# Performance work log

Measured on AMD Instinct MI355X. Metric: run time of the kernel, lower is better.

Reference implementation:

```python
import jax, jax.numpy as jnp
import numpy as np

SC = 11  # window stride / block size; unfold kernel = 3*SC = 33, padding = SC


def _unfold3(x, sc):
    """Equivalent of nn.Unfold(kernel=3*sc, stride=sc, padding=sc) on [b,c,H,W]
    where H, W are multiples of sc. Returns [b, c, 9*sc*sc, n_windows].
    Patch ordering within K differs from torch by a fixed permutation, which is
    immaterial: all contractions over K (mask, softmax, value aggregation) are
    permutation-invariant as long as the same unfold is used everywhere."""
    b, c, H, W = x.shape
    h_sc, w_sc = H // sc, W // sc
    xp = jnp.pad(x, ((0, 0), (0, 0), (sc, sc), (sc, sc)))
    blk = xp.reshape(b, c, h_sc + 2, sc, w_sc + 2, sc)
    # 3x3 neighborhood of sc-blocks around each window
    pat = jnp.stack([blk[:, :, di:di + h_sc, :, dj:dj + w_sc, :]
                     for di in range(3) for dj in range(3)], axis=2)
    # [b,c,9,h_sc,r,w_sc,s] -> [b,c,9,r,s,h_sc,w_sc] -> [b,c,9*sc*sc,n]
    pat = pat.transpose(0, 1, 2, 4, 6, 3, 5)
    return pat.reshape(b, c, 9 * sc * sc, h_sc * w_sc)


def _block_q(x, sc):
    """view(b,c,h_sc,sc,w_sc,sc).permute(0,1,2,4,3,5) -> [b,c,n,sc*sc]"""
    b, c, H, W = x.shape
    h_sc, w_sc = H // sc, W // sc
    y = x.reshape(b, c, h_sc, sc, w_sc, sc).transpose(0, 1, 2, 4, 3, 5)
    return y.reshape(b, c, h_sc * w_sc, sc * sc)


def setup_inputs() -> dict:
    key = jax.random.key(0)
    k1, k2, k3, k4, k5, k6 = jax.random.split(key, 6)
    b, c, h, w = 2, 64, 256, 256
    s = 1.0 / np.sqrt(c)
    return {
        "x_key": jax.random.normal(k1, (b, c, h, w), jnp.float32),
        "x_ref": jax.random.normal(k2, (b, c, h, w), jnp.float32),
        "Wq": jax.random.normal(k3, (c, c), jnp.float32) * s,
        "Wk": jax.random.normal(k4, (c, c), jnp.float32) * s,
        "Wv": jax.random.normal(k5, (c, c), jnp.float32) * s,
        "gamma": jax.random.normal(k6, (1,), jnp.float32) * 0.1,
    }


def reference(x_key, x_ref, Wq, Wk, Wv, gamma):
    sc = SC
    b, c, h_in, w_in = x_key.shape
    x_pad = sc - w_in % sc
    y_pad = sc - h_in % sc
    pad = ((0, 0), (0, 0), (0, y_pad), (0, x_pad))
    fk = jnp.pad(x_key, pad)
    fr = jnp.pad(x_ref, pad)
    b, c, h, w = fk.shape
    h_sc, w_sc = h // sc, w // sc

    # validity mask -> additive attention bias (out-of-image keys penalized)
    fm = jnp.pad(jnp.ones((1, 1, h_in, w_in), fk.dtype), pad)
    fm_k = _unfold3(fm, sc)          # [1,1,K,n]
    fm_q = _block_q(fm, sc)          # [1,1,n,s]
    am = (jnp.einsum('bckn,bcns->bkns', fm_k, fm_q) - 1.0) * 99.0  # [1,K,n,s]

    scale = c ** (-0.5)
    q = jnp.einsum('oi,bihw->bohw', Wq, fk)
    k = jnp.einsum('oi,bihw->bohw', Wk, fr)
    v = jnp.einsum('oi,bihw->bohw', Wv, fr)

    k_u = _unfold3(k, sc) * scale    # [b,c,K,n]
    q_b = _block_q(q, sc)            # [b,c,n,s]
    attn = jnp.einsum('bckn,bcns->bkns', k_u, q_b) + am  # [b,K,n,s]
    attn = jax.nn.softmax(attn, axis=1)

    v_u = _unfold3(v, sc)            # [b,c,K,n]
    r = jnp.einsum('bkns,bckn->bcns', attn, v_u)  # [b,c,n,s]
    r = r.reshape(b, c, h_sc, w_sc, sc, sc).transpose(0, 1, 2, 4, 3, 5)
    r = r.reshape(b, c, h, w)[:, :, :h_in, :w_in]
    return x_ref + r * gamma[0]
```

## Files before the change

### kernel.cpp

```cpp
#include <hip/hip_runtime.h>


typedef unsigned short ushort_t;
typedef unsigned int   uint32;
typedef unsigned long long uint64;
typedef __attribute__((ext_vector_type(8))) short short8;
typedef __attribute__((ext_vector_type(4))) float f32x4;

#define MFMA16(a,b,c) __builtin_amdgcn_mfma_f32_16x16x32_bf16(a,b,c,0,0,0)

#if __has_builtin(__builtin_amdgcn_exp2f)
#define EXP2(x) __builtin_amdgcn_exp2f(x)
#else
#define EXP2(x) exp2f(x)
#endif
#if __has_builtin(__builtin_amdgcn_rcpf)
#define RCP(x) __builtin_amdgcn_rcpf(x)
#else
#define RCP(x) (1.0f/(x))
#endif

#define QPKT_OFF   0u
#define KPKT_OFF   18874368u
#define VPKT_OFF   37748736u

__device__ __forceinline__ ushort_t f2bf(float f){
  uint32 u = __float_as_uint(f);
  u = (u + 0x7FFFu + ((u >> 16) & 1u)) >> 16;
  return (ushort_t)u;
}

__device__ __forceinline__ uint32 pkbf(float a, float b){
#if __has_builtin(__builtin_amdgcn_cvt_pk_bf16_f32)
  typedef __attribute__((ext_vector_type(2))) __bf16 bf2;
  union { bf2 v; uint32 u; } c;
  c.v = __builtin_amdgcn_cvt_pk_bf16_f32(a, b);
  return c.u;
#else
  return (uint32)f2bf(a) | ((uint32)f2bf(b) << 16);
#endif
}

__device__ __forceinline__ void storeK8(ushort_t* __restrict__ base, int nt, int t,
                                        int l15, int h, f32x4 a){
  uint32 lo = pkbf(a[0], a[1]);
  uint32 hi = pkbf(a[2], a[3]);
  int lanep = l15 + 16*((2*t + (h>>1)) & 3);
  size_t off = (size_t)((nt*2 + (t>>1))*64 + lanep)*16 + 8*(h&1);
  *(uint2*)((char*)base + off) = make_uint2(lo, hi);
}

__device__ __forceinline__ short8 ldWfrag(const float* __restrict__ W, int t, int ks,
                                          int l15, int h, float scale){
  const float* p = W + (16*t + l15)*64 + 32*ks + 8*h;
  float4 a = *(const float4*)p;
  float4 b = *(const float4*)(p + 4);
  union { uint4 u; short8 s; } x;
  x.u.x = pkbf(a.x*scale, a.y*scale);
  x.u.y = pkbf(a.z*scale, a.w*scale);
  x.u.z = pkbf(b.x*scale, b.y*scale);
  x.u.w = pkbf(b.z*scale, b.w*scale);
  return x.s;
}

__global__ __launch_bounds__(256) void proj_kernel(
    const float* __restrict__ xk, const float* __restrict__ xr,
    const float* __restrict__ Wq, const float* __restrict__ Wk, const float* __restrict__ Wv,
    ushort_t* __restrict__ qpkt, ushort_t* __restrict__ kpkt, ushort_t* __restrict__ vpkt)
{
  __shared__ __align__(16) float sX[64*192];
  const int tid = threadIdx.x;
  const int lane = tid & 63, wv = tid >> 6;
  const int l15 = lane & 15, h = lane >> 4;
  const int bid = blockIdx.x;
  const bool isQ = bid >= 1152;
  const int id = isQ ? bid - 1152 : bid;
  const int b = id / 576, rem = id % 576, ty = rem / 24, tx = rem % 24;
  const float* xs = (isQ ? xk : xr) + (size_t)b*64*65536;
  const int oy = ty*11, ox = tx*11;
  const int ox3 = ox & 3, xa = ox - ox3;

  #pragma unroll
  for (int i = tid; i < 1024; i += 256) sX[(i>>4)*192 + 176 + (i&15)] = 0.f;

  {
    const int ch = tid >> 2, seg = tid & 3;
    const float* rowp = xs + (size_t)ch*65536 + (size_t)oy*256 + (xa + 4*seg);
    float* sdst = sX + ch*192 + 4*seg;
    if (ty < 23 && tx < 23){
      #pragma unroll
      for (int y = 0; y < 11; ++y)
        *(float4*)(sdst + y*16) = *(const float4*)(rowp + y*256);
    } else {
      const int xg = xa + 4*seg;
      #pragma unroll
      for (int y = 0; y < 11; ++y){
        const bool rk = (oy + y) < 256;
        float4 v;
        v.x = (rk && xg+0 < 256) ? rowp[y*256+0] : 0.f;
        v.y = (rk && xg+1 < 256) ? rowp[y*256+1] : 0.f;
        v.z = (rk && xg+2 < 256) ? rowp[y*256+2] : 0.f;
        v.w = (rk && xg+3 < 256) ? rowp[y*256+3] : 0.f;
        *(float4*)(sdst + y*16) = v;
      }
    }
  }
  __syncthreads();

  const f32x4 zero = {0.f, 0.f, 0.f, 0.f};
  #define XFL(nt, ks, dst) { \
    const int px_ = 16*(nt) + l15; \
    const int y_ = (px_*745) >> 13; \
    const float* pp_ = sX + (32*(ks) + 8*h)*192 + y_*16 + (px_ - y_*11) + ox3; \
    union { uint4 u; short8 s; } r_; \
    r_.u.x = pkbf(pp_[0],    pp_[192]); \
    r_.u.y = pkbf(pp_[384],  pp_[576]); \
    r_.u.z = pkbf(pp_[768],  pp_[960]); \
    r_.u.w = pkbf(pp_[1152], pp_[1344]); \
    dst = r_.s; }

  if (!isQ){
    short8 wkf[4][2], wvf[4][2];
    #pragma unroll
    for (int t = 0; t < 4; ++t){
      wkf[t][0] = ldWfrag(Wk, t, 0, l15, h, 1.f);  wkf[t][1] = ldWfrag(Wk, t, 1, l15, h, 1.f);
      wvf[t][0] = ldWfrag(Wv, t, 0, l15, h, 1.f);  wvf[t][1] = ldWfrag(Wv, t, 1, l15, h, 1.f);
    }
    ushort_t* kb = kpkt + (size_t)id*8192;
    ushort_t* vb = vpkt + (size_t)id*8192;
    const int nt0 = 2*wv, nt1 = 2*wv + 1;
    short8 xf0[2], xf1[2];
    XFL(nt0, 0, xf0[0]); XFL(nt0, 1, xf0[1]);
    XFL(nt1, 0, xf1[0]); XFL(nt1, 1, xf1[1]);
    #pragma unroll
    for (int t = 0; t < 4; ++t){
      f32x4 ak0 = MFMA16(wkf[t][0], xf0[0], zero); ak0 = MFMA16(wkf[t][1], xf0[1], ak0);
      f32x4 ak1 = MFMA16(wkf[t][0], xf1[0], zero); ak1 = MFMA16(wkf[t][1], xf1[1], ak1);
      f32x4 av0 = MFMA16(xf0[0], wvf[t][0], zero); av0 = MFMA16(xf0[1], wvf[t][1], av0);
      f32x4 av1 = MFMA16(xf1[0], wvf[t][0], zero); av1 = MFMA16(xf1[1], wvf[t][1], av1);
      storeK8(kb, nt0, t, l15, h, ak0);
      storeK8(kb, nt1, t, l15, h, ak1);
      uint4 pv;
      pv.x = pkbf(av0[0], av0[1]); pv.y = pkbf(av0[2], av0[3]);
      pv.z = pkbf(av1[0], av1[1]); pv.w = pkbf(av1[2], av1[3]);
      *(uint4*)((char*)vb + (size_t)((wv*4 + t)*64 + lane)*16) = pv;
    }
  } else {
    const float C1 = 0.18033688011112042f;
    short8 wqf[4][2];
    #pragma unroll
    for (int t = 0; t < 4; ++t){
      wqf[t][0] = ldWfrag(Wq, t, 0, l15, h, C1);  wqf[t][1] = ldWfrag(Wq, t, 1, l15, h, C1);
    }
    ushort_t* qb = qpkt + (size_t)id*8192;
    #pragma unroll
    for (int nn = 0; nn < 2; ++nn){
      const int nt = 2*wv + nn;
      short8 xf[2];
      XFL(nt, 0, xf[0]); XFL(nt, 1, xf[1]);
      #pragma unroll
      for (int t = 0; t < 4; ++t){
        f32x4 aq = MFMA16(wqf[t][0], xf[0], zero); aq = MFMA16(wqf[t][1], xf[1], aq);
        storeK8(qb, nt, t, l15, h, aq);
      }
    }
  }
  #undef XFL
}

__global__ __launch_bounds__(128) void attn_kernel(
    ushort_t* qpkt,
    const ushort_t* __restrict__ kpkt, const ushort_t* __restrict__ vpkt,
    const float* __restrict__ gamma)
{
  __shared__ __align__(16) char smem[32768];
  const int tid = threadIdx.x;
  const int lane = tid & 63, wave = tid >> 6;
  const int win = (blockIdx.x & 7)*144 + (blockIdx.x >> 3);
  const int b = win / 576, wid = win % 576, wy = wid / 24, wx = wid % 24;
  const int l15 = lane & 15, h = lane >> 4;

  short8 qf[4][2];
  {
    const ushort_t* qblk = qpkt + (size_t)win*8192;
    #pragma unroll
    for (int mt = 0; mt < 4; ++mt){
      qf[mt][0] = *(const short8*)(qblk + (size_t)(((4*wave+mt)*2 + 0)*64 + lane)*8);
      qf[mt][1] = *(const short8*)(qblk + (size_t)(((4*wave+mt)*2 + 1)*64 + lane)*8);
    }
  }

  uint64 cks = 0; int nv = 0;
  #pragma unroll
  for (int ck = 0; ck < 9; ++ck){
    const int ty = wy - 1 + ck/3, tx = wx - 1 + ck%3;
    if ((unsigned)ty < 24u && (unsigned)tx < 24u){
      cks |= ((uint64)ck) << (4*nv); ++nv;
    }
  }
  const int nu = 2*nv;

  f32x4 o[4][4];
  float lsum[4] = {0.f, 0.f, 0.f, 0.f};
  #pragma unroll
  for (int mt = 0; mt < 4; ++mt)
    #pragma unroll
    for (int u = 0; u < 4; ++u) o[mt][u] = (f32x4){0.f,0.f,0.f,0.f};
  const f32x4 zz = {0.f,0.f,0.f,0.f};

  const ushort_t* gsrcbase = wave ? vpkt : kpkt;
  const int ldsw = wave ? 8192 : 0;

  #define STAGE(u, bu) { \
    const int t_ = (u) >> 1, hf_ = (u) & 1; \
    const int ck_ = (int)((cks >> (4*t_)) & 15); \
    const int cy_ = (ck_*11) >> 5; \
    const int ty_ = wy - 1 + cy_, tx_ = wx - 1 + (ck_ - 3*cy_); \
    const char* g_ = (const char*)(gsrcbase + (size_t)(b*576 + ty_*24 + tx_)*8192) \
                     + hf_*8192 + lane*16; \
    char* l_ = smem + (bu)*16384 + ldsw; \
    _Pragma("unroll") \
    for (int i_ = 0; i_ < 8; ++i_) \
      __builtin_amdgcn_global_load_lds( \
        (const __attribute__((address_space(1))) uint32*)(g_ + i_*1024), \
        (__attribute__((address_space(3))) uint32*)(l_ + i_*1024), 16, 0, 0); \
  }

  STAGE(0, 0);
  STAGE(1, 1);

  #pragma unroll 1
  for (int u = 0; u < nu; ++u){
    const int bu = u & 1;
    if (u + 1 < nu) { __asm__ volatile("s_waitcnt vmcnt(8)" ::: "memory"); }
    else            { __asm__ volatile("s_waitcnt vmcnt(0)" ::: "memory"); }
    __builtin_amdgcn_s_barrier();
    __asm__ volatile("" ::: "memory");

    const int t = u >> 1, hf = u & 1;
    const int ckv = (int)((cks >> (4*t)) & 15);
    const int cyv = (ckv*11) >> 5;
    const int tyv = wy - 1 + cyv, txv = wx - 1 + (ckv - 3*cyv);
    const bool ey = (tyv == 23), ex = (txv == 23);
    const char* lk = smem + bu*16384;
    const char* lv = lk + 8192;

    #pragma unroll
    for (int ntpl = 0; ntpl < 2; ++ntpl){
      const int ntp = 2*hf + ntpl;
      short8 kf00 = *(const short8*)(lk + ((4*ntpl+0)*64 + lane)*16);
      short8 kf01 = *(const short8*)(lk + ((4*ntpl+1)*64 + lane)*16);
      short8 kf10 = *(const short8*)(lk + ((4*ntpl+2)*64 + lane)*16);
      short8 kf11 = *(const short8*)(lk + ((4*ntpl+3)*64 + lane)*16);
      short8 vf0  = *(const short8*)(lv + ((4*ntpl+0)*64 + lane)*16);
      short8 vf1  = *(const short8*)(lv + ((4*ntpl+1)*64 + lane)*16);
      short8 vf2  = *(const short8*)(lv + ((4*ntpl+2)*64 + lane)*16);
      short8 vf3  = *(const short8*)(lv + ((4*ntpl+3)*64 + lane)*16);

      bool okk[8];
      #pragma unroll
      for (int kt = 0; kt < 2; ++kt)
        #pragma unroll
        for (int r = 0; r < 4; ++r){
          const int kl = 32*ntp + 16*kt + 4*h + r;
          bool ok = kl < 121;
          if (ey | ex){
            const int ky = (kl*745) >> 13, kx = kl - ky*11;
            if (ey) ok = ok && (ky < 3);
            if (ex) ok = ok && (kx < 3);
          }
          okk[4*kt + r] = ok;
        }

      #pragma unroll
      for (int mt = 0; mt < 4; ++mt){
        f32x4 s0 = MFMA16(kf00, qf[mt][0], zz); s0 = MFMA16(kf01, qf[mt][1], s0);
        f32x4 s1 = MFMA16(kf10, qf[mt][0], zz); s1 = MFMA16(kf11, qf[mt][1], s1);
        float p[8];
        #pragma unroll
        for (int r = 0; r < 4; ++r){
          p[r]   = okk[r]   ? EXP2(s0[r]) : 0.f;
          p[4+r] = okk[4+r] ? EXP2(s1[r]) : 0.f;
        }
        lsum[mt] += ((p[0]+p[1]) + (p[2]+p[3])) + ((p[4]+p[5]) + (p[6]+p[7]));
        union { uint4 uu; short8 s; } af;
        af.uu.x = pkbf(p[0], p[1]); af.uu.y = pkbf(p[2], p[3]);
        af.uu.z = pkbf(p[4], p[5]); af.uu.w = pkbf(p[6], p[7]);
        o[mt][0] = MFMA16(af.s, vf0, o[mt][0]);
        o[mt][1] = MFMA16(af.s, vf1, o[mt][1]);
        o[mt][2] = MFMA16(af.s, vf2, o[mt][2]);
        o[mt][3] = MFMA16(af.s, vf3, o[mt][3]);
      }
    }

    __asm__ volatile("" ::: "memory");
    __builtin_amdgcn_s_barrier();
    if (u + 2 < nu) STAGE(u + 2, bu);
  }
  #undef STAGE

  const float gm = gamma[0];
  ushort_t* rb = qpkt + (size_t)win*8192 + (size_t)wave*4096;
  #pragma unroll
  for (int mt = 0; mt < 4; ++mt){
    float v = lsum[mt];
    v += __shfl_xor(v, 16); v += __shfl_xor(v, 32);
    #pragma unroll
    for (int r = 0; r < 4; ++r){
      const float den = __shfl(v, 4*h + r);
      const float wg = gm * RCP(den);
      const int qs = 16*mt + 4*h + r;
      #pragma unroll
      for (int u = 0; u < 4; ++u)
        rb[(size_t)qs*64 + 16*u + l15] = f2bf(wg * o[mt][u][r]);
    }
  }
}

__global__ __launch_bounds__(256) void ep_kernel(
    const float* __restrict__ xref, const ushort_t* __restrict__ rbuf,
    float* __restrict__ out)
{
  __shared__ float tile[64][65];
  const int tid = threadIdx.x;
  const int bidx = blockIdx.x;
  const int xc = bidx & 3, y = (bidx >> 2) & 255, b = bidx >> 10;
  const int wy = (y*745) >> 13, qy = y - wy*11;
  {
    const int ch = tid & 63, xs4 = tid >> 6;
    #pragma unroll
    for (int xi = 0; xi < 16; ++xi){
      const int xl = xi*4 + xs4;
      const int x = xc*64 + xl;
      const int wx = (x*745) >> 13, qx = x - wx*11;
      const size_t ridx = (size_t)(b*576 + wy*24 + wx)*8192 + (size_t)(qy*11 + qx)*64 + ch;
      tile[xl][ch] = __uint_as_float(((uint32)rbuf[ridx]) << 16);
    }
  }
  __syncthreads();
  {
    const int xl = tid & 63, cg = tid >> 6;
    const size_t base = (size_t)b*4194304 + (size_t)y*256 + xc*64 + xl;
    #pragma unroll
    for (int ci = 0; ci < 16; ++ci){
      const int c2 = ci*4 + cg;
      const size_t idx = base + (size_t)c2*65536;
      out[idx] = xref[idx] + tile[xl][c2];
    }
  }
}

extern "C" void kernel_launch(void* const* d_in, const int* in_sizes, int n_in,
                              void* d_out, int out_size, void* d_ws, size_t ws_size,
                              hipStream_t stream)
{
  const float* xk = (const float*)d_in[0];
  const float* xr = (const float*)d_in[1];
  const float* Wq = (const float*)d_in[2];
  const float* Wk = (const float*)d_in[3];
  const float* Wv = (const float*)d_in[4];
  const float* gm = (const float*)d_in[5];
  float* out = (float*)d_out;
  char* ws = (char*)d_ws;
  ushort_t* qp = (ushort_t*)(ws + QPKT_OFF);
  ushort_t* kp = (ushort_t*)(ws + KPKT_OFF);
  ushort_t* vp = (ushort_t*)(ws + VPKT_OFF);
  (void)in_sizes; (void)n_in; (void)out_size; (void)ws_size;

  proj_kernel<<<2304, 256, 0, stream>>>(xk, xr, Wq, Wk, Wv, qp, kp, vp);
  attn_kernel<<<1152, 128, 0, stream>>>(qp, kp, vp, gm);
  ep_kernel<<<2048, 256, 0, stream>>>(xr, qp, out);
}
```

Before: 251.1 us.

## Split attention key tiles across four waves and reduce partial outputs via LDS

The attention kernel moves from 2 to 4 waves per window. Each wave pair handles half of the query rows and half of the key sub-tiles per stage, and the partial outputs and row sums are merged through shared memory at the end. The validity mask becomes an additive bias fed in as the MFMA accumulator init, and row sums are computed with an extra MFMA against a ones vector instead of scalar adds. This aims to raise latency hiding and cut per-wave VALU work, at the cost of an extra LDS reduction with several block barriers and an additional MFMA per tile.

```diff
diff --git a/kernel.cpp b/kernel.cpp
--- a/kernel.cpp
+++ b/kernel.cpp
@@ -168,7 +168,7 @@
   #undef XFL
 }
 
-__global__ __launch_bounds__(128) void attn_kernel(
+__global__ __launch_bounds__(256) void attn_kernel(
     ushort_t* qpkt,
     const ushort_t* __restrict__ kpkt, const ushort_t* __restrict__ vpkt,
     const float* __restrict__ gamma)
@@ -176,6 +176,7 @@
   __shared__ __align__(16) char smem[32768];
   const int tid = threadIdx.x;
   const int lane = tid & 63, wave = tid >> 6;
+  const int qh = wave & 1, kh = wave >> 1;
   const int win = (blockIdx.x & 7)*144 + (blockIdx.x >> 3);
   const int b = win / 576, wid = win % 576, wy = wid / 24, wx = wid % 24;
   const int l15 = lane & 15, h = lane >> 4;
@@ -185,8 +186,8 @@
     const ushort_t* qblk = qpkt + (size_t)win*8192;
     #pragma unroll
     for (int mt = 0; mt < 4; ++mt){
-      qf[mt][0] = *(const short8*)(qblk + (size_t)(((4*wave+mt)*2 + 0)*64 + lane)*8);
-      qf[mt][1] = *(const short8*)(qblk + (size_t)(((4*wave+mt)*2 + 1)*64 + lane)*8);
+      qf[mt][0] = *(const short8*)(qblk + (size_t)(((4*qh+mt)*2 + 0)*64 + lane)*8);
+      qf[mt][1] = *(const short8*)(qblk + (size_t)(((4*qh+mt)*2 + 1)*64 + lane)*8);
     }
   }
 
@@ -200,27 +201,34 @@
   }
   const int nu = 2*nv;
 
-  f32x4 o[4][4];
-  float lsum[4] = {0.f, 0.f, 0.f, 0.f};
+  const f32x4 zz = {0.f,0.f,0.f,0.f};
+  f32x4 o[4][4], lsumC[4];
   #pragma unroll
-  for (int mt = 0; mt < 4; ++mt)
-    #pragma unroll
-    for (int u = 0; u < 4; ++u) o[mt][u] = (f32x4){0.f,0.f,0.f,0.f};
-  const f32x4 zz = {0.f,0.f,0.f,0.f};
-
-  const ushort_t* gsrcbase = wave ? vpkt : kpkt;
-  const int ldsw = wave ? 8192 : 0;
+  for (int mt = 0; mt < 4; ++mt){
+    lsumC[mt] = zz;
+    #pragma unroll
+    for (int u = 0; u < 4; ++u) o[mt][u] = zz;
+  }
+  f32x4 init_i;
+  #pragma unroll
+  for (int r = 0; r < 4; ++r) init_i[r] = (4*h + r >= 9) ? -1.0e4f : 0.f;
+  short8 ones;
+  #pragma unroll
+  for (int j = 0; j < 8; ++j) ones[j] = (short)0x3F80;
+
+  const ushort_t* gsrc = (wave < 2) ? kpkt : vpkt;
+  const int ldsoff = (wave >> 1)*8192 + (wave & 1)*4096;
 
   #define STAGE(u, bu) { \
     const int t_ = (u) >> 1, hf_ = (u) & 1; \
     const int ck_ = (int)((cks >> (4*t_)) & 15); \
     const int cy_ = (ck_*11) >> 5; \
     const int ty_ = wy - 1 + cy_, tx_ = wx - 1 + (ck_ - 3*cy_); \
-    const char* g_ = (const char*)(gsrcbase + (size_t)(b*576 + ty_*24 + tx_)*8192) \
-                     + hf_*8192 + lane*16; \
-    char* l_ = smem + (bu)*16384 + ldsw; \
+    const char* g_ = (const char*)(gsrc + (size_t)(b*576 + ty_*24 + tx_)*8192) \
+                     + hf_*8192 + (wave & 1)*4096 + lane*16; \
+    char* l_ = smem + (bu)*16384 + ldsoff + lane*16; \
     _Pragma("unroll") \
-    for (int i_ = 0; i_ < 8; ++i_) \
+    for (int i_ = 0; i_ < 4; ++i_) \
       __builtin_amdgcn_global_load_lds( \
         (const __attribute__((address_space(1))) uint32*)(g_ + i_*1024), \
         (__attribute__((address_space(3))) uint32*)(l_ + i_*1024), 16, 0, 0); \
@@ -232,7 +240,7 @@
   #pragma unroll 1
   for (int u = 0; u < nu; ++u){
     const int bu = u & 1;
-    if (u + 1 < nu) { __asm__ volatile("s_waitcnt vmcnt(8)" ::: "memory"); }
+    if (u + 1 < nu) { __asm__ volatile("s_waitcnt vmcnt(4)" ::: "memory"); }
     else            { __asm__ volatile("s_waitcnt vmcnt(0)" ::: "memory"); }
     __builtin_amdgcn_s_barrier();
     __asm__ volatile("" ::: "memory");
@@ -242,55 +250,56 @@
     const int cyv = (ckv*11) >> 5;
     const int tyv = wy - 1 + cyv, txv = wx - 1 + (ckv - 3*cyv);
     const bool ey = (tyv == 23), ex = (txv == 23);
-    const char* lk = smem + bu*16384;
-    const char* lv = lk + 8192;
-
-    #pragma unroll
-    for (int ntpl = 0; ntpl < 2; ++ntpl){
-      const int ntp = 2*hf + ntpl;
-      short8 kf00 = *(const short8*)(lk + ((4*ntpl+0)*64 + lane)*16);
-      short8 kf01 = *(const short8*)(lk + ((4*ntpl+1)*64 + lane)*16);
-      short8 kf10 = *(const short8*)(lk + ((4*ntpl+2)*64 + lane)*16);
-      short8 kf11 = *(const short8*)(lk + ((4*ntpl+3)*64 + lane)*16);
-      short8 vf0  = *(const short8*)(lv + ((4*ntpl+0)*64 + lane)*16);
-      short8 vf1  = *(const short8*)(lv + ((4*ntpl+1)*64 + lane)*16);
-      short8 vf2  = *(const short8*)(lv + ((4*ntpl+2)*64 + lane)*16);
-      short8 vf3  = *(const short8*)(lv + ((4*ntpl+3)*64 + lane)*16);
-
-      bool okk[8];
-      #pragma unroll
-      for (int kt = 0; kt < 2; ++kt)
+    const int ntp = 2*hf + kh;
+
+    f32x4 b0, b1;
+    if (ey | ex){
+      #pragma unroll
+      for (int kt = 0; kt < 2; ++kt){
+        f32x4 bb;
         #pragma unroll
         for (int r = 0; r < 4; ++r){
           const int kl = 32*ntp + 16*kt + 4*h + r;
-          bool ok = kl < 121;
-          if (ey | ex){
-            const int ky = (kl*745) >> 13, kx = kl - ky*11;
-            if (ey) ok = ok && (ky < 3);
-            if (ex) ok = ok && (kx < 3);
-          }
-          okk[4*kt + r] = ok;
+          const int ky = (kl*745) >> 13, kx = kl - ky*11;
+          bool ok = (kl < 121) && (!ey || ky < 3) && (!ex || kx < 3);
+          bb[r] = ok ? 0.f : -1.0e4f;
         }
-
-      #pragma unroll
-      for (int mt = 0; mt < 4; ++mt){
-        f32x4 s0 = MFMA16(kf00, qf[mt][0], zz); s0 = MFMA16(kf01, qf[mt][1], s0);
-        f32x4 s1 = MFMA16(kf10, qf[mt][0], zz); s1 = MFMA16(kf11, qf[mt][1], s1);
-        float p[8];
-        #pragma unroll
-        for (int r = 0; r < 4; ++r){
-          p[r]   = okk[r]   ? EXP2(s0[r]) : 0.f;
-          p[4+r] = okk[4+r] ? EXP2(s1[r]) : 0.f;
-        }
-        lsum[mt] += ((p[0]+p[1]) + (p[2]+p[3])) + ((p[4]+p[5]) + (p[6]+p[7]));
-        union { uint4 uu; short8 s; } af;
-        af.uu.x = pkbf(p[0], p[1]); af.uu.y = pkbf(p[2], p[3]);
-        af.uu.z = pkbf(p[4], p[5]); af.uu.w = pkbf(p[6], p[7]);
-        o[mt][0] = MFMA16(af.s, vf0, o[mt][0]);
-        o[mt][1] = MFMA16(af.s, vf1, o[mt][1]);
-        o[mt][2] = MFMA16(af.s, vf2, o[mt][2]);
-        o[mt][3] = MFMA16(af.s, vf3, o[mt][3]);
-      }
+        if (kt) b1 = bb; else b0 = bb;
+      }
+    } else {
+      b0 = zz;
+      b1 = (hf & kh) ? init_i : zz;
+    }
+
+    const char* lk = smem + bu*16384 + kh*4096;
+    const char* lv = smem + bu*16384 + 8192 + kh*4096;
+    short8 kf00 = *(const short8*)(lk + (0*64 + lane)*16);
+    short8 kf01 = *(const short8*)(lk + (1*64 + lane)*16);
+    short8 kf10 = *(const short8*)(lk + (2*64 + lane)*16);
+    short8 kf11 = *(const short8*)(lk + (3*64 + lane)*16);
+    short8 vf0  = *(const short8*)(lv + (0*64 + lane)*16);
+    short8 vf1  = *(const short8*)(lv + (1*64 + lane)*16);
+    short8 vf2  = *(const short8*)(lv + (2*64 + lane)*16);
+    short8 vf3  = *(const short8*)(lv + (3*64 + lane)*16);
+
+    #pragma unroll
+    for (int mt = 0; mt < 4; ++mt){
+      f32x4 s0 = MFMA16(kf00, qf[mt][0], b0); s0 = MFMA16(kf01, qf[mt][1], s0);
+      f32x4 s1 = MFMA16(kf10, qf[mt][0], b1); s1 = MFMA16(kf11, qf[mt][1], s1);
+      float p[8];
+      #pragma unroll
+      for (int r = 0; r < 4; ++r){
+        p[r]   = EXP2(s0[r]);
+        p[4+r] = EXP2(s1[r]);
+      }
+      union { uint4 uu; short8 s; } af;
+      af.uu.x = pkbf(p[0], p[1]); af.uu.y = pkbf(p[2], p[3]);
+      af.uu.z = pkbf(p[4], p[5]); af.uu.w = pkbf(p[6], p[7]);
+      o[mt][0] = MFMA16(af.s, vf0, o[mt][0]);
+      o[mt][1] = MFMA16(af.s, vf1, o[mt][1]);
+      o[mt][2] = MFMA16(af.s, vf2, o[mt][2]);
+      o[mt][3] = MFMA16(af.s, vf3, o[mt][3]);
+      lsumC[mt] = MFMA16(af.s, ones, lsumC[mt]);
     }
 
     __asm__ volatile("" ::: "memory");
@@ -299,20 +308,59 @@
   }
   #undef STAGE
 
-  const float gm = gamma[0];
-  ushort_t* rb = qpkt + (size_t)win*8192 + (size_t)wave*4096;
-  #pragma unroll
-  for (int mt = 0; mt < 4; ++mt){
-    float v = lsum[mt];
-    v += __shfl_xor(v, 16); v += __shfl_xor(v, 32);
-    #pragma unroll
-    for (int r = 0; r < 4; ++r){
-      const float den = __shfl(v, 4*h + r);
-      const float wg = gm * RCP(den);
-      const int qs = 16*mt + 4*h + r;
-      #pragma unroll
-      for (int u = 0; u < 4; ++u)
-        rb[(size_t)qs*64 + 16*u + l15] = f2bf(wg * o[mt][u][r]);
+  __syncthreads();
+  {
+    float* base = (float*)(smem + qh*12288);
+    if (kh){
+      #pragma unroll
+      for (int mt = 0; mt < 4; ++mt){
+        *(f32x4*)(base + (mt*2+0)*256 + lane*4) = o[mt][0];
+        *(f32x4*)(base + (mt*2+1)*256 + lane*4) = o[mt][1];
+        *(f32x4*)(base + (8+mt)*256 + lane*4)   = lsumC[mt];
+      }
+    }
+  }
+  __syncthreads();
+  if (!kh){
+    float* base = (float*)(smem + qh*12288);
+    #pragma unroll
+    for (int mt = 0; mt < 4; ++mt){
+      o[mt][0] += *(const f32x4*)(base + (mt*2+0)*256 + lane*4);
+      o[mt][1] += *(const f32x4*)(base + (mt*2+1)*256 + lane*4);
+      lsumC[mt] += *(const f32x4*)(base + (8+mt)*256 + lane*4);
+    }
+  }
+  __syncthreads();
+  {
+    float* base2 = (float*)(smem + qh*8192);
+    if (kh){
+      #pragma unroll
+      for (int mt = 0; mt < 4; ++mt){
+        *(f32x4*)(base2 + (mt*2+0)*256 + lane*4) = o[mt][2];
+        *(f32x4*)(base2 + (mt*2+1)*256 + lane*4) = o[mt][3];
+      }
+    }
+  }
+  __syncthreads();
+  if (!kh){
+    float* base2 = (float*)(smem + qh*8192);
+    #pragma unroll
+    for (int mt = 0; mt < 4; ++mt){
+      o[mt][2] += *(const f32x4*)(base2 + (mt*2+0)*256 + lane*4);
+      o[mt][3] += *(const f32x4*)(base2 + (mt*2+1)*256 + lane*4);
+    }
+    const float gm = gamma[0];
+    ushort_t* rb = qpkt + (size_t)win*8192 + (size_t)qh*4096;
+    #pragma unroll
+    for (int mt = 0; mt < 4; ++mt){
+      #pragma unroll
+      for (int r = 0; r < 4; ++r){
+        const float wg = gm * RCP(lsumC[mt][r]);
+        const int qs = 16*mt + 4*h + r;
+        #pragma unroll
+        for (int u = 0; u < 4; ++u)
+          rb[(size_t)qs*64 + 16*u + l15] = f2bf(wg * o[mt][u][r]);
+      }
     }
   }
 }
@@ -368,6 +416,6 @@
   (void)in_sizes; (void)n_in; (void)out_size; (void)ws_size;
 
   proj_kernel<<<2304, 256, 0, stream>>>(xk, xr, Wq, Wk, Wv, qp, kp, vp);
-  attn_kernel<<<1152, 128, 0, stream>>>(qp, kp, vp, gm);
+  attn_kernel<<<1152, 256, 0, stream>>>(qp, kp, vp, gm);
   ep_kernel<<<2048, 256, 0, stream>>>(xr, qp, out);
 }
```

Result: faster. 236.5 us (-5.8%).
